# Performance work log

Hardware: AMD Instinct MI355X
Metric: run time of the kernel (lower is better)

Reference implementation:

```python
import jax, jax.numpy as jnp
import numpy as np

B, T, D, H, C = 32, 160, 512, 256, 6625  # batch, time, feat, gru hidden, num classes


def _gru_scan(x_proj, rk, rbias):
    """Keras GRU (reset_after=True) over time.
    x_proj: [T, B, 3H] = x @ kernel + input_bias (precomputed).
    rk: [H, 3H] recurrent kernel, rbias: [3H] recurrent bias.
    Returns hidden states [T, B, H]."""
    h0 = jnp.zeros((x_proj.shape[1], rk.shape[0]), dtype=x_proj.dtype)

    def step(h, xp):
        inner = h @ rk + rbias                 # [B, 3H]
        xz, xr, xh = jnp.split(xp, 3, axis=-1)
        rz, rr, rh = jnp.split(inner, 3, axis=-1)
        z = jax.nn.sigmoid(xz + rz)            # update gate
        r = jax.nn.sigmoid(xr + rr)            # reset gate
        hh = jnp.tanh(xh + r * rh)             # candidate
        hn = z * h + (1.0 - z) * hh
        return hn, hn

    _, hs = jax.lax.scan(step, h0, x_proj)
    return hs  # [T, B, H]


def setup_inputs() -> dict:
    key = jax.random.key(0)
    ks = jax.random.split(key, 9)
    s_in, s_rec, s_cls = 1.0 / np.sqrt(D), 1.0 / np.sqrt(H), 0.1
    return {
        "x": jax.random.normal(ks[0], (B, T, D), jnp.float32),
        "kernel_fwd": jax.random.normal(ks[1], (D, 3 * H), jnp.float32) * s_in,
        "rk_fwd": jax.random.normal(ks[2], (H, 3 * H), jnp.float32) * s_rec,
        "bias_fwd": jnp.zeros((2, 3 * H), jnp.float32),
        "kernel_bwd": jax.random.normal(ks[3], (D, 3 * H), jnp.float32) * s_in,
        "rk_bwd": jax.random.normal(ks[4], (H, 3 * H), jnp.float32) * s_rec,
        "bias_bwd": jnp.zeros((2, 3 * H), jnp.float32),
        "W": jax.random.truncated_normal(ks[5], -2.0, 2.0, (2 * H, C), jnp.float32) * s_cls,
        "b": jnp.zeros((C,), jnp.float32),
    }


def reference(x, kernel_fwd, rk_fwd, bias_fwd, kernel_bwd, rk_bwd, bias_bwd, W, b):
    x_t = jnp.transpose(x, (1, 0, 2))                       # [T, B, D]
    # forward direction
    xp_f = x_t @ kernel_fwd + bias_fwd[0]                   # [T, B, 3H]
    h_f = _gru_scan(xp_f, rk_fwd, bias_fwd[1])              # [T, B, H]
    # backward direction: run on time-reversed input, reverse output
    x_rev = x_t[::-1]
    xp_b = x_rev @ kernel_bwd + bias_bwd[0]
    h_b = _gru_scan(xp_b, rk_bwd, bias_bwd[1])[::-1]        # [T, B, H]
    out = jnp.concatenate([h_f, h_b], axis=-1)              # [T, B, 2H]
    # classifier applied per position; original reshape/matmul/reshape/transpose
    # ([B,T,2H]->[-1,2H]@W -> [B,T,C] -> [T,B,C]) is equivalent to this:
    logits = out @ W + b                                    # [T, B, C]
    return logits
```

## Files before the change

### kernel.cpp

```cpp
#include <hip/hip_runtime.h>
#include <hip/hip_bf16.h>


#define B 32
#define T 160
#define D 512
#define H 256
#define C 6625
#define H3 768
#define NT16 416
#define KP_PER_DIR 393216
#define RKB_PER_DIR 196608

typedef __attribute__((ext_vector_type(8))) short short8v;
typedef __attribute__((ext_vector_type(4))) float float4v;

__device__ inline unsigned short f2bf(float v) {
    __hip_bfloat16 b = __float2bfloat16(v);
    return *reinterpret_cast<unsigned short*>(&b);
}
__device__ inline float bf2f(unsigned short u) {
    return __uint_as_float((unsigned int)u << 16);
}

__global__ __launch_bounds__(256) void pack_rkB_kernel(
    const float* __restrict__ rkf, const float* __restrict__ rkb,
    unsigned short* __restrict__ rkB)
{
    const int idx = blockIdx.x * 256 + threadIdx.x;
    const int dir = blockIdx.y;
    const float* rk = dir ? rkb : rkf;
    const int i   = idx & 7;
    const int col = (idx >> 3) & 15;
    const int kc  = (idx >> 7) & 31;
    const int nt  = idx >> 12;
    rkB[dir * RKB_PER_DIR + idx] = f2bf(rk[(kc * 8 + i) * H3 + nt * 16 + col]);
}

__global__ __launch_bounds__(256) void pack_W_kernel(
    const float* __restrict__ W, unsigned short* __restrict__ Wp)
{
    const int idx = blockIdx.x * 256 + threadIdx.x;
    const int i   = idx & 7;
    const int col = (idx >> 3) & 15;
    const int kc  = (idx >> 7) & 63;
    const int nt  = idx >> 13;
    const int k = kc * 8 + i;
    const int c = nt * 16 + col;
    const float v = (c < C) ? W[k * C + c] : 0.f;
    Wp[idx] = f2bf(v);
}

__global__ __launch_bounds__(256) void pack_xb_kernel(
    const float* __restrict__ x, unsigned short* __restrict__ xb)
{
    const int idx = blockIdx.x * 256 + threadIdx.x;
    const int k   = idx & 511;
    const int row = idx >> 9;
    const int t   = row >> 5;
    const int b   = row & 31;
    xb[idx] = f2bf(x[(b * T + t) * 512 + k]);
}

__global__ __launch_bounds__(256) void pack_kern_kernel(
    const float* __restrict__ kf, const float* __restrict__ kb,
    unsigned short* __restrict__ kernP)
{
    const int idx = blockIdx.x * 256 + threadIdx.x;
    const int dir = blockIdx.y;
    const float* kern = dir ? kb : kf;
    const int i   = idx & 7;
    const int col = (idx >> 3) & 15;
    const int kc  = (idx >> 7) & 63;
    const int nt  = idx >> 13;
    kernP[dir * KP_PER_DIR + idx] = f2bf(kern[(kc * 8 + i) * H3 + nt * 16 + col]);
}

__global__ __launch_bounds__(256) void proj_mfma_kernel(
    const unsigned short* __restrict__ xb,
    const unsigned short* __restrict__ kernP,
    const float* __restrict__ bias_f,
    const float* __restrict__ bias_b,
    unsigned short* __restrict__ xpb)
{
    const int bid = blockIdx.x;
    const int ct  = bid / 40;
    const int rt  = bid % 40;
    const int dir = blockIdx.y;
    const int lane = threadIdx.x & 63;
    const int wid  = threadIdx.x >> 6;
    const int wm = wid >> 1, wn = wid & 1;
    const int rowBase = rt * 128 + wm * 64;
    const int lrow = lane & 15;
    const int lk8  = lane >> 4;
    const float* bias = dir ? bias_b : bias_f;

    float4v acc[4][4];
#pragma unroll
    for (int i = 0; i < 4; ++i)
#pragma unroll
        for (int k = 0; k < 4; ++k) acc[i][k] = (float4v){0.f, 0.f, 0.f, 0.f};

    const short* A  = (const short*)xb;
    const short* Bp = (const short*)(kernP + dir * KP_PER_DIR);
    const int ntBase = ct * 8 + wn * 4;

    int arow[4];
#pragma unroll
    for (int mt = 0; mt < 4; ++mt) {
        const int r0 = rowBase + mt * 16;
        const int s  = r0 >> 5;
        arow[mt] = (dir ? (159 - s) : s) * 32 + (r0 & 31);
    }

    for (int k0 = 0; k0 < 512; k0 += 32) {
        short8v aF[4], bF[4];
#pragma unroll
        for (int mt = 0; mt < 4; ++mt)
            aF[mt] = *(const short8v*)&A[(arow[mt] + lrow) * 512 + k0 + lk8 * 8];
#pragma unroll
        for (int ntw = 0; ntw < 4; ++ntw)
            bF[ntw] = *(const short8v*)&Bp[((ntBase + ntw) * 64 + (k0 >> 3) + lk8) * 128 + lrow * 8];
#pragma unroll
        for (int mt = 0; mt < 4; ++mt)
#pragma unroll
            for (int ntw = 0; ntw < 4; ++ntw)
                acc[mt][ntw] = __builtin_amdgcn_mfma_f32_16x16x32_bf16(
                    aF[mt], bF[ntw], acc[mt][ntw], 0, 0, 0);
    }

    const int orow = (lane >> 4) * 4;
#pragma unroll
    for (int ntw = 0; ntw < 4; ++ntw) {
        const int c = (ntBase + ntw) * 16 + lrow;
        const float bc = bias[c];
#pragma unroll
        for (int mt = 0; mt < 4; ++mt)
#pragma unroll
            for (int v = 0; v < 4; ++v)
                xpb[(size_t)(dir * 5120 + rowBase + mt * 16 + orow + v) * H3 + c]
                    = f2bf(acc[mt][ntw][v] + bc);
    }
}

__global__ __launch_bounds__(768, 3) void gru_scan_v6(
    const unsigned short* __restrict__ xpb,
    const unsigned short* __restrict__ rkB,
    const float* __restrict__ bias_f,
    const float* __restrict__ bias_b,
    __hip_bfloat16* __restrict__ hcatb)
{
    const int bid = blockIdx.x;
    const int dir = bid >> 5;
    const int b   = bid & 31;
    const int tid = threadIdx.x;
    const int wv  = tid >> 6;
    const int lane = tid & 63;
    const int lrow = lane & 15;
    const int lk8  = lane >> 4;
    const int j   = tid & 255;
    const float* bias = dir ? bias_b : bias_f;
    const short* Bp = (const short*)(rkB + (size_t)dir * RKB_PER_DIR);

    short8v bw[32];
#pragma unroll
    for (int i = 0; i < 4; ++i)
#pragma unroll
        for (int kk = 0; kk < 8; ++kk)
            bw[i * 8 + kk] = *(const short8v*)
                &Bp[(((wv * 4 + i) * 32) + kk * 4 + lk8) * 128 + lrow * 8];

    float rbz = 0.f, rbr = 0.f, rbh = 0.f;
    if (tid < 256) {
        rbz = bias[H3 + j];
        rbr = bias[H3 + 256 + j];
        rbh = bias[H3 + 512 + j];
    }

    __shared__ float hfp[256];
    __shared__ __align__(16) unsigned short hus[256];
    __shared__ float sums[768];
    if (tid < 256) { hfp[tid] = 0.f; hus[tid] = 0; }
    __syncthreads();

    for (int s = 0; s < T; ++s) {
        float xz = 0.f, xr = 0.f, xh = 0.f;
        if (tid < 256) {
            const unsigned short* xrow = xpb + ((size_t)(dir * T + s) * B + b) * H3;
            xz = bf2f(xrow[j]);
            xr = bf2f(xrow[256 + j]);
            xh = bf2f(xrow[512 + j]);
        }

        float4v a0 = {0.f,0.f,0.f,0.f}, a1 = {0.f,0.f,0.f,0.f};
        float4v a2 = {0.f,0.f,0.f,0.f}, a3 = {0.f,0.f,0.f,0.f};
#pragma unroll
        for (int kk = 0; kk < 8; ++kk) {
            short8v aF = *(const short8v*)&hus[kk * 32 + lk8 * 8];
            a0 = __builtin_amdgcn_mfma_f32_16x16x32_bf16(aF, bw[0 * 8 + kk], a0, 0, 0, 0);
            a1 = __builtin_amdgcn_mfma_f32_16x16x32_bf16(aF, bw[1 * 8 + kk], a1, 0, 0, 0);
            a2 = __builtin_amdgcn_mfma_f32_16x16x32_bf16(aF, bw[2 * 8 + kk], a2, 0, 0, 0);
            a3 = __builtin_amdgcn_mfma_f32_16x16x32_bf16(aF, bw[3 * 8 + kk], a3, 0, 0, 0);
        }
        if (lane < 16) {
            sums[(wv * 4 + 0) * 16 + lane] = a0[0];
            sums[(wv * 4 + 1) * 16 + lane] = a1[0];
            sums[(wv * 4 + 2) * 16 + lane] = a2[0];
            sums[(wv * 4 + 3) * 16 + lane] = a3[0];
        }
        __syncthreads();

        if (tid < 256) {
            const float sz = sums[j];
            const float sr = sums[256 + j];
            const float sh = sums[512 + j];
            const float z  = 1.f / (1.f + __expf(-(xz + sz + rbz)));
            const float r  = 1.f / (1.f + __expf(-(xr + sr + rbr)));
            const float pre = xh + r * (sh + rbh);
            const float e2  = __expf(2.f * pre);
            const float hh  = 1.f - 2.f / (e2 + 1.f);
            const float hn  = z * hfp[j] + (1.f - z) * hh;
            hfp[j] = hn;
            hus[j] = f2bf(hn);
            const int ta = dir ? (T - 1 - s) : s;
            hcatb[(ta * B + b) * 512 + dir * 256 + j] = __float2bfloat16(hn);
        }
        __syncthreads();
    }
}

__global__ __launch_bounds__(256) void cls_mfma3_kernel(
    const unsigned short* __restrict__ hcatb,
    const unsigned short* __restrict__ Wp,
    const float* __restrict__ bias,
    float* __restrict__ out)
{
    const int bid = blockIdx.x;
    const int ctn = bid / 80;
    const int rt  = bid % 80;
    const int tid = threadIdx.x;
    const int lane = tid & 63;
    const int wid  = tid >> 6;
    const int wm = wid >> 1, wn = wid & 1;
    const int lrow = lane & 15;
    const int lk8  = lane >> 4;
    const int r0   = rt * 64;

    __shared__ __align__(16) unsigned short As[64 * 512];

    {
        const uint4* src = (const uint4*)hcatb;
        for (int it = 0; it < 16; ++it) {
            const int v   = it * 256 + tid;
            const int row = v >> 6;
            const int c16 = (v & 63) << 4;
            const uint4 d = src[(size_t)(r0 + row) * 64 + (v & 63)];
            *(uint4*)((char*)As + row * 1024 + (c16 ^ ((row & 7) << 4))) = d;
        }
    }
    __syncthreads();

    float4v acc[2][8];
#pragma unroll
    for (int i = 0; i < 2; ++i)
#pragma unroll
        for (int k = 0; k < 8; ++k) acc[i][k] = (float4v){0.f, 0.f, 0.f, 0.f};

    const short* Bp = (const short*)Wp;
    const int ntBase = ctn * 16 + wn * 8;

    for (int k0 = 0; k0 < 512; k0 += 32) {
        short8v aF[2], bF[8];
#pragma unroll
        for (int mt = 0; mt < 2; ++mt) {
            const int row = wm * 32 + mt * 16 + lrow;
            const int cb  = (k0 * 2 + lk8 * 16) ^ ((row & 7) << 4);
            aF[mt] = *(const short8v*)((const char*)As + row * 1024 + cb);
        }
#pragma unroll
        for (int ntw = 0; ntw < 8; ++ntw)
            bF[ntw] = *(const short8v*)&Bp[((ntBase + ntw) * 64 + (k0 >> 3) + lk8) * 128 + lrow * 8];
#pragma unroll
        for (int mt = 0; mt < 2; ++mt)
#pragma unroll
            for (int ntw = 0; ntw < 8; ++ntw)
                acc[mt][ntw] = __builtin_amdgcn_mfma_f32_16x16x32_bf16(
                    aF[mt], bF[ntw], acc[mt][ntw], 0, 0, 0);
    }

    const int orow = (lane >> 4) * 4;
#pragma unroll
    for (int ntw = 0; ntw < 8; ++ntw) {
        const int c = (ntBase + ntw) * 16 + lrow;
        if (c >= C) continue;
        const float bc = bias[c];
#pragma unroll
        for (int mt = 0; mt < 2; ++mt)
#pragma unroll
            for (int v = 0; v < 4; ++v)
                out[(size_t)(r0 + wm * 32 + mt * 16 + orow + v) * C + c]
                    = acc[mt][ntw][v] + bc;
    }
}

__global__ __launch_bounds__(256) void proj_kernel(
    const float* __restrict__ x, const float* __restrict__ kf,
    const float* __restrict__ kb, const float* __restrict__ bias_f,
    const float* __restrict__ bias_b, float* __restrict__ xp)
{
    const int ct  = blockIdx.x;
    const int s   = blockIdx.y;
    const int dir = blockIdx.z;
    const int tid = threadIdx.x;
    const int t   = dir ? (T - 1 - s) : s;
    const float* kern = dir ? kb : kf;
    const float* bias = dir ? bias_b : bias_f;

    __shared__ float xs[32 * 512];
    for (int it = 0; it < 16; ++it) {
        int v = it * 256 + tid, row = v >> 7, k4 = v & 127;
        *(float4*)&xs[(row << 9) + (k4 << 2)] =
            *(const float4*)&x[((row * T + t) << 9) + (k4 << 2)];
    }
    __syncthreads();

    const int col = ct * 256 + tid;
    float acc[32];
#pragma unroll
    for (int r = 0; r < 32; ++r) acc[r] = 0.f;
    for (int k = 0; k < 512; k += 4) {
        float w0 = kern[(k + 0) * H3 + col];
        float w1 = kern[(k + 1) * H3 + col];
        float w2 = kern[(k + 2) * H3 + col];
        float w3 = kern[(k + 3) * H3 + col];
#pragma unroll
        for (int r = 0; r < 32; ++r) {
            float4 xv = *(const float4*)&xs[(r << 9) + k];
            acc[r] += xv.x * w0 + xv.y * w1 + xv.z * w2 + xv.w * w3;
        }
    }
    const float bb = bias[col];
    for (int r = 0; r < 32; ++r)
        xp[((dir * T + s) * B + r) * H3 + col] = acc[r] + bb;
}

__global__ __launch_bounds__(1024) void gru_scan_f32(
    const float* __restrict__ xp,
    const float* __restrict__ rk_f, const float* __restrict__ rk_b,
    const float* __restrict__ bias_f, const float* __restrict__ bias_b,
    float* __restrict__ hcat)
{
    const int bid = blockIdx.x;
    const int dir = bid >> 5;
    const int b   = bid & 31;
    const int tid = threadIdx.x;
    const int kg  = tid >> 8;
    const int j   = tid & 255;
    const int k0  = kg << 6;
    const float* rk   = dir ? rk_b : rk_f;
    const float* bias = dir ? bias_b : bias_f;
    const float rbz = bias[H3 + j];
    const float rbr = bias[H3 + 256 + j];
    const float rbh = bias[H3 + 512 + j];

    __shared__ float h[256];
    __shared__ float part[3][4][256];
    if (tid < 256) h[tid] = 0.f;
    __syncthreads();

    for (int s = 0; s < T; ++s) {
        const float* xrow = xp + ((dir * T + s) * B + b) * H3;
        float az = 0.f, ar = 0.f, ah = 0.f;
#pragma unroll 4
        for (int k = k0; k < k0 + 64; k += 4) {
            float4 h4 = *(const float4*)&h[k];
            const float* rkp = rk + k * H3 + j;
            az += h4.x * rkp[0];       ar += h4.x * rkp[256];       ah += h4.x * rkp[512];
            az += h4.y * rkp[H3];      ar += h4.y * rkp[H3+256];    ah += h4.y * rkp[H3+512];
            az += h4.z * rkp[2*H3];    ar += h4.z * rkp[2*H3+256];  ah += h4.z * rkp[2*H3+512];
            az += h4.w * rkp[3*H3];    ar += h4.w * rkp[3*H3+256];  ah += h4.w * rkp[3*H3+512];
        }
        part[0][kg][j] = az; part[1][kg][j] = ar; part[2][kg][j] = ah;
        __syncthreads();
        if (tid < 256) {
            const float sz = part[0][0][tid]+part[0][1][tid]+part[0][2][tid]+part[0][3][tid];
            const float sr = part[1][0][tid]+part[1][1][tid]+part[1][2][tid]+part[1][3][tid];
            const float sh = part[2][0][tid]+part[2][1][tid]+part[2][2][tid]+part[2][3][tid];
            const float xz = xrow[tid], xr = xrow[256+tid], xh = xrow[512+tid];
            const float z  = 1.f / (1.f + __expf(-(xz + sz + rbz)));
            const float r  = 1.f / (1.f + __expf(-(xr + sr + rbr)));
            const float pre = xh + r * (sh + rbh);
            const float e2  = __expf(2.f * pre);
            const float hh  = 1.f - 2.f / (e2 + 1.f);
            const float hn  = z * h[tid] + (1.f - z) * hh;
            h[tid] = hn;
            const int ta = dir ? (T - 1 - s) : s;
            hcat[(ta * B + b) * (2 * H) + dir * H + tid] = hn;
        }
        __syncthreads();
    }
}

__global__ __launch_bounds__(256) void cls_f32_kernel(
    const float* __restrict__ hcat, const float* __restrict__ W,
    const float* __restrict__ bias, float* __restrict__ out)
{
    const int bid = blockIdx.x;
    const int ct  = bid / 160;
    const int rt  = bid % 160;
    const int tid = threadIdx.x;
    const int r0  = rt * 32;

    __shared__ float hs[32 * 512];
    for (int it = 0; it < 16; ++it) {
        int v = it * 256 + tid, row = v >> 7, k4 = v & 127;
        *(float4*)&hs[(row << 9) + (k4 << 2)] =
            *(const float4*)&hcat[((r0 + row) << 9) + (k4 << 2)];
    }
    __syncthreads();

    const int c0 = ct * 512 + tid;
    const int c1 = c0 + 256;
    const bool v1 = (c1 < C);
    float acc0[32], acc1[32];
#pragma unroll
    for (int r = 0; r < 32; ++r) { acc0[r] = 0.f; acc1[r] = 0.f; }
    for (int k = 0; k < 512; k += 4) {
        const float* wp = W + k * C;
        float w00 = wp[c0], w01 = wp[C+c0], w02 = wp[2*C+c0], w03 = wp[3*C+c0];
        float w10 = v1 ? wp[c1] : 0.f, w11 = v1 ? wp[C+c1] : 0.f;
        float w12 = v1 ? wp[2*C+c1] : 0.f, w13 = v1 ? wp[3*C+c1] : 0.f;
#pragma unroll
        for (int r = 0; r < 32; ++r) {
            float4 hv = *(const float4*)&hs[(r << 9) + k];
            acc0[r] += hv.x*w00 + hv.y*w01 + hv.z*w02 + hv.w*w03;
            acc1[r] += hv.x*w10 + hv.y*w11 + hv.z*w12 + hv.w*w13;
        }
    }
    const float b0 = bias[c0];
    const float b1 = v1 ? bias[c1] : 0.f;
    for (int r = 0; r < 32; ++r) {
        out[(size_t)(r0+r)*C + c0] = acc0[r] + b0;
        if (v1) out[(size_t)(r0+r)*C + c1] = acc1[r] + b1;
    }
}

extern "C" void kernel_launch(void* const* d_in, const int* in_sizes, int n_in,
                              void* d_out, int out_size, void* d_ws, size_t ws_size,
                              hipStream_t stream) {
    const float* x     = (const float*)d_in[0];
    const float* kf    = (const float*)d_in[1];
    const float* rkf   = (const float*)d_in[2];
    const float* biasf = (const float*)d_in[3];
    const float* kb    = (const float*)d_in[4];
    const float* rkb   = (const float*)d_in[5];
    const float* biasb = (const float*)d_in[6];
    const float* W     = (const float*)d_in[7];
    const float* bvec  = (const float*)d_in[8];
    float* out = (float*)d_out;

    const size_t rkB_bytes   = (size_t)2 * RKB_PER_DIR * 2;
    const size_t Wp_bytes    = (size_t)NT16 * 8192 * 2;
    const size_t hcatb_bytes = (size_t)T * B * 2 * H * 2;
    const size_t planA_bytes = rkB_bytes + Wp_bytes + hcatb_bytes;

    unsigned short* xpb   = (unsigned short*)out;
    unsigned short* xb    = (unsigned short*)((char*)out + (size_t)2 * 5120 * H3 * 4);
    unsigned short* kernP = (unsigned short*)((char*)xb + (size_t)5120 * 512 * 2);

    if (ws_size >= planA_bytes) {
        char* wsb = (char*)d_ws;
        unsigned short* rkB   = (unsigned short*)wsb;
        unsigned short* Wp    = (unsigned short*)(wsb + rkB_bytes);
        __hip_bfloat16* hcatb = (__hip_bfloat16*)(wsb + rkB_bytes + Wp_bytes);

        pack_rkB_kernel<<<dim3(768, 2), 256, 0, stream>>>(rkf, rkb, rkB);
        pack_W_kernel<<<13312, 256, 0, stream>>>(W, Wp);
        pack_xb_kernel<<<10240, 256, 0, stream>>>(x, xb);
        pack_kern_kernel<<<dim3(1536, 2), 256, 0, stream>>>(kf, kb, kernP);

        proj_mfma_kernel<<<dim3(240, 2), 256, 0, stream>>>(xb, kernP, biasf, biasb, xpb);

        gru_scan_v6<<<64, 768, 0, stream>>>(xpb, rkB, biasf, biasb, hcatb);

        cls_mfma3_kernel<<<2080, 256, 0, stream>>>((const unsigned short*)hcatb,
                                                   Wp, bvec, out);
    } else {
        float* xp   = out;
        float* hcat = (float*)d_ws;
        dim3 g1(3, T, 2);
        proj_kernel<<<g1, 256, 0, stream>>>(x, kf, kb, biasf, biasb, xp);
        gru_scan_f32<<<64, 1024, 0, stream>>>(xp, rkf, rkb, biasf, biasb, hcat);
        cls_f32_kernel<<<13 * 160, 256, 0, stream>>>(hcat, W, bvec, out);
    }
}
```

Measured before the change: 299.1 us.

## Process four batch rows per GRU scan block using MFMA rows

The recurrent scan kernel now handles four batch elements per block instead of one, filling MFMA rows 0-3 (lrow&3) with separate hidden states so the register-resident recurrent weights are reused across four sequences. The grid shrinks from 64 to 16 blocks, and each update thread computes gates for four batch elements. This removes redundant weight loads and MFMA work per batch row. The trade-off is fewer blocks on the GPU and more serial gate arithmetic per thread inside each timestep.

```diff
diff --git a/kernel.cpp b/kernel.cpp
--- a/kernel.cpp
+++ b/kernel.cpp
@@ -11,6 +11,7 @@
 #define NT16 416
 #define KP_PER_DIR 393216
 #define RKB_PER_DIR 196608
+#define HUS_STRIDE 272
 
 typedef __attribute__((ext_vector_type(8))) short short8v;
 typedef __attribute__((ext_vector_type(4))) float float4v;
@@ -143,7 +144,7 @@
     }
 }
 
-__global__ __launch_bounds__(768, 3) void gru_scan_v6(
+__global__ __launch_bounds__(768, 3) void gru_scan_v8(
     const unsigned short* __restrict__ xpb,
     const unsigned short* __restrict__ rkB,
     const float* __restrict__ bias_f,
@@ -151,8 +152,8 @@
     __hip_bfloat16* __restrict__ hcatb)
 {
     const int bid = blockIdx.x;
-    const int dir = bid >> 5;
-    const int b   = bid & 31;
+    const int dir = bid >> 3;
+    const int bg  = bid & 7;
     const int tid = threadIdx.x;
     const int wv  = tid >> 6;
     const int lane = tid & 63;
@@ -177,53 +178,71 @@
         rbh = bias[H3 + 512 + j];
     }
 
-    __shared__ float hfp[256];
-    __shared__ __align__(16) unsigned short hus[256];
-    __shared__ float sums[768];
-    if (tid < 256) { hfp[tid] = 0.f; hus[tid] = 0; }
+    __shared__ __align__(16) unsigned short hus[4 * HUS_STRIDE];
+    __shared__ float hfp[256 * 4];
+    __shared__ float sums[768 * 4];
+    for (int v = tid; v < 4 * HUS_STRIDE; v += 768) hus[v] = 0;
+    for (int v = tid; v < 1024; v += 768) hfp[v] = 0.f;
     __syncthreads();
 
+    const int batBase = bg * 4;
+
     for (int s = 0; s < T; ++s) {
-        float xz = 0.f, xr = 0.f, xh = 0.f;
+        float xg[3][4];
         if (tid < 256) {
-            const unsigned short* xrow = xpb + ((size_t)(dir * T + s) * B + b) * H3;
-            xz = bf2f(xrow[j]);
-            xr = bf2f(xrow[256 + j]);
-            xh = bf2f(xrow[512 + j]);
+            const size_t rowb = (size_t)((dir * T + s) * 32 + batBase) * H3;
+#pragma unroll
+            for (int g = 0; g < 3; ++g)
+#pragma unroll
+                for (int b = 0; b < 4; ++b)
+                    xg[g][b] = bf2f(xpb[rowb + (size_t)b * H3 + g * 256 + j]);
         }
 
         float4v a0 = {0.f,0.f,0.f,0.f}, a1 = {0.f,0.f,0.f,0.f};
         float4v a2 = {0.f,0.f,0.f,0.f}, a3 = {0.f,0.f,0.f,0.f};
 #pragma unroll
         for (int kk = 0; kk < 8; ++kk) {
-            short8v aF = *(const short8v*)&hus[kk * 32 + lk8 * 8];
+            short8v aF = *(const short8v*)
+                &hus[(lrow & 3) * HUS_STRIDE + kk * 32 + lk8 * 8];
             a0 = __builtin_amdgcn_mfma_f32_16x16x32_bf16(aF, bw[0 * 8 + kk], a0, 0, 0, 0);
             a1 = __builtin_amdgcn_mfma_f32_16x16x32_bf16(aF, bw[1 * 8 + kk], a1, 0, 0, 0);
             a2 = __builtin_amdgcn_mfma_f32_16x16x32_bf16(aF, bw[2 * 8 + kk], a2, 0, 0, 0);
             a3 = __builtin_amdgcn_mfma_f32_16x16x32_bf16(aF, bw[3 * 8 + kk], a3, 0, 0, 0);
         }
         if (lane < 16) {
-            sums[(wv * 4 + 0) * 16 + lane] = a0[0];
-            sums[(wv * 4 + 1) * 16 + lane] = a1[0];
-            sums[(wv * 4 + 2) * 16 + lane] = a2[0];
-            sums[(wv * 4 + 3) * 16 + lane] = a3[0];
+            *(float4v*)&sums[((wv * 4 + 0) * 16 + lrow) * 4] = a0;
+            *(float4v*)&sums[((wv * 4 + 1) * 16 + lrow) * 4] = a1;
+            *(float4v*)&sums[((wv * 4 + 2) * 16 + lrow) * 4] = a2;
+            *(float4v*)&sums[((wv * 4 + 3) * 16 + lrow) * 4] = a3;
         }
         __syncthreads();
 
         if (tid < 256) {
-            const float sz = sums[j];
-            const float sr = sums[256 + j];
-            const float sh = sums[512 + j];
-            const float z  = 1.f / (1.f + __expf(-(xz + sz + rbz)));
-            const float r  = 1.f / (1.f + __expf(-(xr + sr + rbr)));
-            const float pre = xh + r * (sh + rbh);
-            const float e2  = __expf(2.f * pre);
-            const float hh  = 1.f - 2.f / (e2 + 1.f);
-            const float hn  = z * hfp[j] + (1.f - z) * hh;
-            hfp[j] = hn;
-            hus[j] = f2bf(hn);
+            const float4 zv = *(const float4*)&sums[j * 4];
+            const float4 rv = *(const float4*)&sums[(256 + j) * 4];
+            const float4 hv = *(const float4*)&sums[(512 + j) * 4];
+            float4 hold = *(const float4*)&hfp[j * 4];
+            float hn[4];
+            const float* zp = &zv.x; const float* rp = &rv.x;
+            const float* hp = &hv.x; const float* op = &hold.x;
+#pragma unroll
+            for (int b = 0; b < 4; ++b) {
+                const float z  = 1.f / (1.f + __expf(-(xg[0][b] + zp[b] + rbz)));
+                const float r  = 1.f / (1.f + __expf(-(xg[1][b] + rp[b] + rbr)));
+                const float pre = xg[2][b] + r * (hp[b] + rbh);
+                const float e2  = __expf(2.f * pre);
+                const float th  = 1.f - 2.f / (e2 + 1.f);
+                hn[b] = z * op[b] + (1.f - z) * th;
+            }
+            *(float4*)&hfp[j * 4] = make_float4(hn[0], hn[1], hn[2], hn[3]);
+#pragma unroll
+            for (int b = 0; b < 4; ++b)
+                hus[b * HUS_STRIDE + j] = f2bf(hn[b]);
             const int ta = dir ? (T - 1 - s) : s;
-            hcatb[(ta * B + b) * 512 + dir * 256 + j] = __float2bfloat16(hn);
+            __hip_bfloat16* hrow = hcatb + (size_t)(ta * 32 + batBase) * 512 + dir * 256 + j;
+#pragma unroll
+            for (int b = 0; b < 4; ++b)
+                hrow[(size_t)b * 512] = __float2bfloat16(hn[b]);
         }
         __syncthreads();
     }
@@ -481,7 +500,7 @@
 
         proj_mfma_kernel<<<dim3(240, 2), 256, 0, stream>>>(xb, kernP, biasf, biasb, xpb);
 
-        gru_scan_v6<<<64, 768, 0, stream>>>(xpb, rkB, biasf, biasb, hcatb);
+        gru_scan_v8<<<16, 768, 0, stream>>>(xpb, rkB, biasf, biasb, hcatb);
 
         cls_mfma3_kernel<<<2080, 256, 0, stream>>>((const unsigned short*)hcatb,
                                                    Wp, bvec, out);
```

Result: slower. 411.5 us (+37.6%).

## Remap GRU scan so each wave owns matching z/r/h columns, drop one barrier

Applied to the files above, without the earlier changes.

The recurrent scan now runs 16 waves of 1024 threads, and each wave computes the z, r and candidate gate columns for the same 16 hidden units. The gate math can then run directly from the MFMA accumulators without the shared-memory sums exchange and its extra __syncthreads per timestep. The hidden state is double-buffered in LDS and kept in registers, so only one barrier per step remains. In exchange, only 16 lanes per wave do the elementwise work, and the larger block may raise register pressure.

```diff
diff --git a/kernel.cpp b/kernel.cpp
--- a/kernel.cpp
+++ b/kernel.cpp
@@ -143,7 +143,7 @@
     }
 }
 
-__global__ __launch_bounds__(768, 3) void gru_scan_v6(
+__global__ __launch_bounds__(1024) void gru_scan_v9(
     const unsigned short* __restrict__ xpb,
     const unsigned short* __restrict__ rkB,
     const float* __restrict__ bias_f,
@@ -158,72 +158,61 @@
     const int lane = tid & 63;
     const int lrow = lane & 15;
     const int lk8  = lane >> 4;
-    const int j   = tid & 255;
     const float* bias = dir ? bias_b : bias_f;
     const short* Bp = (const short*)(rkB + (size_t)dir * RKB_PER_DIR);
 
-    short8v bw[32];
-#pragma unroll
-    for (int i = 0; i < 4; ++i)
+    short8v bw[3][8];
+#pragma unroll
+    for (int g = 0; g < 3; ++g)
 #pragma unroll
         for (int kk = 0; kk < 8; ++kk)
-            bw[i * 8 + kk] = *(const short8v*)
-                &Bp[(((wv * 4 + i) * 32) + kk * 4 + lk8) * 128 + lrow * 8];
-
-    float rbz = 0.f, rbr = 0.f, rbh = 0.f;
-    if (tid < 256) {
-        rbz = bias[H3 + j];
-        rbr = bias[H3 + 256 + j];
-        rbh = bias[H3 + 512 + j];
-    }
-
-    __shared__ float hfp[256];
-    __shared__ __align__(16) unsigned short hus[256];
-    __shared__ float sums[768];
-    if (tid < 256) { hfp[tid] = 0.f; hus[tid] = 0; }
+            bw[g][kk] = *(const short8v*)
+                &Bp[(((g * 16 + wv) * 32) + kk * 4 + lk8) * 128 + lrow * 8];
+
+    const int j = wv * 16 + lrow;
+
+    __shared__ __align__(16) unsigned short hus[2][256];
+    __shared__ float rbl[768];
+    if (tid < 256) { hus[0][tid] = 0; hus[1][tid] = 0; }
+    if (tid < 768) rbl[tid] = bias[H3 + tid];
     __syncthreads();
 
+    float h_old = 0.f;
+
     for (int s = 0; s < T; ++s) {
+        const unsigned short* hcur = hus[s & 1];
+
         float xz = 0.f, xr = 0.f, xh = 0.f;
-        if (tid < 256) {
+        if (lane < 16) {
             const unsigned short* xrow = xpb + ((size_t)(dir * T + s) * B + b) * H3;
             xz = bf2f(xrow[j]);
             xr = bf2f(xrow[256 + j]);
             xh = bf2f(xrow[512 + j]);
         }
 
-        float4v a0 = {0.f,0.f,0.f,0.f}, a1 = {0.f,0.f,0.f,0.f};
-        float4v a2 = {0.f,0.f,0.f,0.f}, a3 = {0.f,0.f,0.f,0.f};
+        float4v a0 = {0.f,0.f,0.f,0.f}, a1 = {0.f,0.f,0.f,0.f}, a2 = {0.f,0.f,0.f,0.f};
 #pragma unroll
         for (int kk = 0; kk < 8; ++kk) {
-            short8v aF = *(const short8v*)&hus[kk * 32 + lk8 * 8];
-            a0 = __builtin_amdgcn_mfma_f32_16x16x32_bf16(aF, bw[0 * 8 + kk], a0, 0, 0, 0);
-            a1 = __builtin_amdgcn_mfma_f32_16x16x32_bf16(aF, bw[1 * 8 + kk], a1, 0, 0, 0);
-            a2 = __builtin_amdgcn_mfma_f32_16x16x32_bf16(aF, bw[2 * 8 + kk], a2, 0, 0, 0);
-            a3 = __builtin_amdgcn_mfma_f32_16x16x32_bf16(aF, bw[3 * 8 + kk], a3, 0, 0, 0);
-        }
+            short8v aF = *(const short8v*)&hcur[kk * 32 + lk8 * 8];
+            a0 = __builtin_amdgcn_mfma_f32_16x16x32_bf16(aF, bw[0][kk], a0, 0, 0, 0);
+            a1 = __builtin_amdgcn_mfma_f32_16x16x32_bf16(aF, bw[1][kk], a1, 0, 0, 0);
+            a2 = __builtin_amdgcn_mfma_f32_16x16x32_bf16(aF, bw[2][kk], a2, 0, 0, 0);
+        }
+
         if (lane < 16) {
-            sums[(wv * 4 + 0) * 16 + lane] = a0[0];
-            sums[(wv * 4 + 1) * 16 + lane] = a1[0];
-            sums[(wv * 4 + 2) * 16 + lane] = a2[0];
-            sums[(wv * 4 + 3) * 16 + lane] = a3[0];
-        }
-        __syncthreads();
-
-        if (tid < 256) {
-            const float sz = sums[j];
-            const float sr = sums[256 + j];
-            const float sh = sums[512 + j];
-            const float z  = 1.f / (1.f + __expf(-(xz + sz + rbz)));
-            const float r  = 1.f / (1.f + __expf(-(xr + sr + rbr)));
-            const float pre = xh + r * (sh + rbh);
+            const float rbz = rbl[j];
+            const float rbr = rbl[256 + j];
+            const float rbh = rbl[512 + j];
+            const float z  = 1.f / (1.f + __expf(-(xz + a0[0] + rbz)));
+            const float r  = 1.f / (1.f + __expf(-(xr + a1[0] + rbr)));
+            const float pre = xh + r * (a2[0] + rbh);
             const float e2  = __expf(2.f * pre);
-            const float hh  = 1.f - 2.f / (e2 + 1.f);
-            const float hn  = z * hfp[j] + (1.f - z) * hh;
-            hfp[j] = hn;
-            hus[j] = f2bf(hn);
+            const float th  = 1.f - 2.f / (e2 + 1.f);
+            const float hn  = z * h_old + (1.f - z) * th;
+            h_old = hn;
+            hus[(s & 1) ^ 1][j] = f2bf(hn);
             const int ta = dir ? (T - 1 - s) : s;
-            hcatb[(ta * B + b) * 512 + dir * 256 + j] = __float2bfloat16(hn);
+            hcatb[(size_t)(ta * B + b) * 512 + dir * 256 + j] = __float2bfloat16(hn);
         }
         __syncthreads();
     }
@@ -481,7 +470,7 @@
 
         proj_mfma_kernel<<<dim3(240, 2), 256, 0, stream>>>(xb, kernP, biasf, biasb, xpb);
 
-        gru_scan_v6<<<64, 768, 0, stream>>>(xpb, rkB, biasf, biasb, hcatb);
+        gru_scan_v9<<<64, 1024, 0, stream>>>(xpb, rkB, biasf, biasb, hcatb);
 
         cls_mfma3_kernel<<<2080, 256, 0, stream>>>((const unsigned short*)hcatb,
                                                    Wp, bvec, out);
```

New measurement: 357.7 us. +19.6%, slower.
